# Kernel tuning notes

Measured on AMD Instinct MI355X. Metric: run time of the kernel, lower is better.

## Reference

```python
import jax, jax.numpy as jnp
import numpy as np

N = 12        # ALL_QUBITS
COM_Q = 9     # COM_QUBITS
IMG_Q = 11    # IMG_QUBITS
LAYERS = 2
SQRT2 = float(np.sqrt(2.0))
H_GATE = jnp.asarray([[1.0, 1.0], [1.0, -1.0]], dtype=jnp.complex64) / SQRT2


def _bitrev_perm(q):
    # column j of the wires-1..q subspace corresponds to param index bitrev(j)
    idx = np.arange(2 ** q)
    rev = np.zeros_like(idx)
    for bpos in range(q):
        rev |= ((idx >> bpos) & 1) << (q - 1 - bpos)
    return rev


def _apply_1q(state, U, w):
    # state: (B, 2^N) complex; apply 2x2 gate U on wire w (wire 0 = MSB)
    B = state.shape[0]
    s = state.reshape(B, 2 ** w, 2, -1)
    return jnp.einsum('ij,bpjq->bpiq', U, s).reshape(B, -1)


def _apply_cnot(state, c, t):
    B = state.shape[0]
    s = state.reshape((B,) + (2,) * N)
    s0 = jax.lax.slice_in_dim(s, 0, 1, axis=c + 1)
    s1 = jnp.flip(jax.lax.slice_in_dim(s, 1, 2, axis=c + 1), axis=t + 1)
    return jnp.concatenate([s0, s1], axis=c + 1).reshape(B, -1)


def _frqi(state, angles, q):
    # Hadamards on wires 1..q, then uniformly-controlled RY(angles) on wire 0
    for w in range(1, q + 1):
        state = _apply_1q(state, H_GATE, w)
    rev = _bitrev_perm(q)
    half = 0.5 * angles[:, rev]            # (B, 2^q), angle per control column
    c = jnp.cos(half)[:, :, None]
    s = jnp.sin(half)[:, :, None]
    B = state.shape[0]
    st = state.reshape(B, 2, 2 ** q, -1)   # (B, wire0, wires1..q, rest)
    new0 = c * st[:, 0] - s * st[:, 1]
    new1 = s * st[:, 0] + c * st[:, 1]
    return jnp.stack([new0, new1], axis=1).reshape(B, -1)


def _rot(phi, theta, omega):
    # PennyLane Rot = RZ(omega) RY(theta) RZ(phi)
    c = jnp.cos(theta / 2)
    s = jnp.sin(theta / 2)
    m00 = jnp.exp(-0.5j * (phi + omega)) * c
    m01 = -jnp.exp(0.5j * (phi - omega)) * s
    m10 = jnp.exp(-0.5j * (phi - omega)) * s
    m11 = jnp.exp(0.5j * (phi + omega)) * c
    return jnp.stack([jnp.stack([m00, m01]), jnp.stack([m10, m11])])


def _circuit(com_params, img_params, qp):
    B = com_params.shape[0]
    state = jnp.zeros((B, 2 ** N), jnp.complex64).at[:, 0].set(1.0)
    state = _frqi(state, com_params, COM_Q)
    for l in range(LAYERS):  # StronglyEntanglingLayers
        for w in range(N):
            state = _apply_1q(state, _rot(qp[l, w, 0], qp[l, w, 1], qp[l, w, 2]), w)
        r = l % (N - 1) + 1  # default ranges
        for w in range(N):
            state = _apply_cnot(state, w, (w + r) % N)
    state = _frqi(state, img_params, IMG_Q)
    p = (jnp.abs(state.reshape(B, 2, -1)) ** 2).sum(axis=2)  # (B, 2) wire-0 probs
    return p[:, 1] - p[:, 0]  # expval of Hamiltonian = -1 * Z(0)


def setup_inputs() -> dict:
    key = jax.random.key(0)
    k1, k2, k3 = jax.random.split(key, 3)
    B = 1024
    x = jax.random.uniform(k1, (B, 2, 32, 32), dtype=jnp.float32)
    W = jax.random.normal(k2, (512, 2048), dtype=jnp.float32) * 0.02
    b = jnp.zeros((512,), dtype=jnp.float32)
    quantum_params = jax.random.uniform(k3, (LAYERS, N, 3), dtype=jnp.float32) * float(np.pi)
    return {"x": x, "W": W, "b": b, "quantum_params": quantum_params}


def reference(x, W, b, quantum_params):
    B = x.shape[0]
    xf = x.reshape(B, -1)                 # (B, 2048) img_params
    com = xf @ W.T + b                    # (B, 512) classical_nn output
    return _circuit(com, xf, quantum_params)
```

## Files before the change

### kernel.cpp

```cpp
#include <hip/hip_runtime.h>
#include <math.h>

#define RS2f 0.70710678118654752f
#define XSTR 4160

typedef __attribute__((ext_vector_type(8))) short bf16x8;
typedef __attribute__((ext_vector_type(4))) float f32x4;

__device__ __forceinline__ unsigned short f2bf(float f) {
    unsigned u = __float_as_uint(f);
    unsigned r = (u + 0x7fffu + ((u >> 16) & 1u)) >> 16;
    return (unsigned short)r;
}
__device__ __forceinline__ float bf2f(unsigned short h) {
    return __uint_as_float(((unsigned)h) << 16);
}

__global__ __launch_bounds__(256) void split_all(const float* __restrict__ x,
                                                 const float* __restrict__ W,
                                                 unsigned short* __restrict__ xc,
                                                 unsigned short* __restrict__ wc) {
    int idx = blockIdx.x * 256 + threadIdx.x;
    const float* src; unsigned short* dst;
    if (idx < 524288) { src = x; dst = xc; }
    else              { idx -= 524288; src = W; dst = wc; }
    int m = idx >> 9;
    int c4 = (idx & 511) << 2;
    const float4 v = *(const float4*)&src[m * 2048 + c4];
    ushort4 hi, lo;
    hi.x = f2bf(v.x); lo.x = f2bf(v.x - bf2f(hi.x));
    hi.y = f2bf(v.y); lo.y = f2bf(v.y - bf2f(hi.y));
    hi.z = f2bf(v.z); lo.z = f2bf(v.z - bf2f(hi.z));
    hi.w = f2bf(v.w); lo.w = f2bf(v.w - bf2f(hi.w));
    *(ushort4*)&dst[(size_t)m * XSTR + c4] = hi;
    *(ushort4*)&dst[(size_t)m * XSTR + 2048 + c4] = lo;
}

__global__ __launch_bounds__(256) void gemm64(const unsigned short* __restrict__ A,
                                              const unsigned short* __restrict__ B,
                                              float* __restrict__ P, int nch) {
    __shared__ short As[64 * 64];
    __shared__ short Bs[64 * 64];
    const int tid = threadIdx.x, lane = tid & 63, wv = tid >> 6;
    const int quad = lane >> 4, mrow = lane & 15;
    const int m0 = blockIdx.x * 64, n0 = blockIdx.y * 64;
    const int kb = blockIdx.z * nch * 64;
    const int lrow = lane >> 3;
    const int gseg = (lane & 7) ^ lrow;

    f32x4 acc[4];
    #pragma unroll
    for (int j = 0; j < 4; ++j) acc[j] = (f32x4){0.f, 0.f, 0.f, 0.f};

    for (int ch = 0; ch < nch; ++ch) {
        const int ko = kb + ch * 64;
        #pragma unroll
        for (int t = 0; t < 2; ++t) {
            const int ra = (wv * 2 + t) * 8;
            const unsigned short* ga = A + (size_t)(m0 + ra + lrow) * XSTR + ko + gseg * 8;
            const unsigned short* gb = B + (size_t)(n0 + ra + lrow) * XSTR + ko + gseg * 8;
            __builtin_amdgcn_global_load_lds(
                (const __attribute__((address_space(1))) void*)ga,
                (__attribute__((address_space(3))) void*)(As + ra * 64), 16, 0, 0);
            __builtin_amdgcn_global_load_lds(
                (const __attribute__((address_space(1))) void*)gb,
                (__attribute__((address_space(3))) void*)(Bs + ra * 64), 16, 0, 0);
        }
        __syncthreads();
        #pragma unroll
        for (int ks = 0; ks < 2; ++ks) {
            const int q = ks * 4 + quad;
            const int am = wv * 16 + mrow;
            bf16x8 af = *(const bf16x8*)&As[am * 64 + ((q ^ (am & 7)) << 3)];
            #pragma unroll
            for (int j = 0; j < 4; ++j) {
                const int bn = j * 16 + mrow;
                bf16x8 bf = *(const bf16x8*)&Bs[bn * 64 + ((q ^ (bn & 7)) << 3)];
                acc[j] = __builtin_amdgcn_mfma_f32_16x16x32_bf16(af, bf, acc[j], 0, 0, 0);
            }
        }
        __syncthreads();
    }
    float* Pz = P + (size_t)blockIdx.z * 524288;
    #pragma unroll
    for (int j = 0; j < 4; ++j)
        #pragma unroll
        for (int r = 0; r < 4; ++r)
            Pz[(m0 + wv * 16 + quad * 4 + r) * 512 + n0 + j * 16 + mrow] = acc[j][r];
}

__global__ __launch_bounds__(256) void reduce_kernel(float* __restrict__ P,
                                                     const float* __restrict__ bias,
                                                     int SK) {
    int i = blockIdx.x * 256 + threadIdx.x;
    float s = bias[i & 511];
    for (int z = 0; z < SK; ++z) s += P[(size_t)z * 524288 + i];
    P[i] = s;
}

__global__ __launch_bounds__(256) void gemm_f32(const float* __restrict__ A,
                                                const float* __restrict__ W,
                                                float* __restrict__ C) {
    __shared__ float Asf[64][33];
    __shared__ float Bsf[32][33];
    const int tid = threadIdx.x;
    const int m0 = blockIdx.x * 64;
    const int n0 = blockIdx.y * 32;
    const int tm = tid >> 4, tn = tid & 15;
    float acc[4][2] = {};
    for (int k0 = 0; k0 < 2048; k0 += 32) {
        #pragma unroll
        for (int i = 0; i < 8; ++i) {
            int idx = tid + i * 256;
            Asf[idx >> 5][idx & 31] = A[(m0 + (idx >> 5)) * 2048 + k0 + (idx & 31)];
        }
        #pragma unroll
        for (int i = 0; i < 4; ++i) {
            int idx = tid + i * 256;
            Bsf[idx >> 5][idx & 31] = W[(n0 + (idx >> 5)) * 2048 + k0 + (idx & 31)];
        }
        __syncthreads();
        #pragma unroll
        for (int kk = 0; kk < 32; ++kk) {
            float a0 = Asf[tm*4+0][kk], a1 = Asf[tm*4+1][kk];
            float a2 = Asf[tm*4+2][kk], a3 = Asf[tm*4+3][kk];
            float b0 = Bsf[tn*2+0][kk], b1 = Bsf[tn*2+1][kk];
            acc[0][0] += a0*b0; acc[0][1] += a0*b1;
            acc[1][0] += a1*b0; acc[1][1] += a1*b1;
            acc[2][0] += a2*b0; acc[2][1] += a2*b1;
            acc[3][0] += a3*b0; acc[3][1] += a3*b1;
        }
        __syncthreads();
    }
    #pragma unroll
    for (int r = 0; r < 4; ++r)
        #pragma unroll
        for (int c = 0; c < 2; ++c)
            C[(m0 + tm*4 + r) * 512 + n0 + tn*2 + c] = acc[r][c];
}

struct CMat { float m00r,m00i,m01r,m01i,m10r,m10i,m11r,m11i; };

__device__ __forceinline__ CMat mk_rot(const float* __restrict__ qp, int l, int w) {
    const float* g = qp + (l * 12 + w) * 3;
    float phi = g[0], th = g[1], om = g[2];
    float st, ct, sa, ca, sb, cb;
    sincosf(0.5f * th, &st, &ct);
    sincosf(0.5f * (phi + om), &sa, &ca);
    sincosf(0.5f * (phi - om), &sb, &cb);
    CMat M;
    M.m00r =  ct * ca; M.m00i = -ct * sa;
    M.m01r = -st * cb; M.m01i = -st * sb;
    M.m10r =  st * cb; M.m10i = -st * sb;
    M.m11r =  ct * ca; M.m11i =  ct * sa;
    return M;
}

template<int W> struct WI {
    static constexpr int kind = (W == 0 || W == 7) ? 2 : ((W >= 1 && W <= 6) ? 1 : 0);
    static constexpr int eb   = (W >= 8) ? (11 - W) : 0;
    static constexpr int lm   = (W >= 1 && W <= 6) ? (1 << (6 - W)) : 0;
    static constexpr int vm   = (W == 0) ? 2 : ((W == 7) ? 1 : 0);
};

__device__ __forceinline__ void exch_put(float* xbuf, int slot,
                                         const float vr[16], const float vi[16]) {
    __syncthreads();
    float4* p = (float4*)xbuf;
    #pragma unroll
    for (int j = 0; j < 8; ++j)
        p[(j << 8) + slot] = make_float4(vr[2*j], vi[2*j], vr[2*j+1], vi[2*j+1]);
    __syncthreads();
}

__device__ __forceinline__ void shfl_perm(float vr[16], float vi[16], int src) {
    #pragma unroll
    for (int e = 0; e < 16; ++e) {
        vr[e] = __shfl(vr[e], src, 64);
        vi[e] = __shfl(vi[e], src, 64);
    }
}

template<int EB>
__device__ __forceinline__ void rot_local(float vr[16], float vi[16], const CMat& M) {
    #pragma unroll
    for (int e = 0; e < 16; ++e) if (!(e & (1 << EB))) {
        const int e1 = e | (1 << EB);
        float x0r = vr[e],  x0i = vi[e];
        float x1r = vr[e1], x1i = vi[e1];
        vr[e]  = M.m00r*x0r - M.m00i*x0i + M.m01r*x1r - M.m01i*x1i;
        vi[e]  = M.m00r*x0i + M.m00i*x0r + M.m01r*x1i + M.m01i*x1r;
        vr[e1] = M.m10r*x0r - M.m10i*x0i + M.m11r*x1r - M.m11i*x1i;
        vi[e1] = M.m10r*x0i + M.m10i*x0r + M.m11r*x1i + M.m11i*x1r;
    }
}

template<int LM>
__device__ __forceinline__ void rot_lane(float vr[16], float vi[16], int lane, const CMat& M) {
    const bool hi = lane & LM;
    const float Ar = hi ? M.m11r : M.m00r, Ai = hi ? M.m11i : M.m00i;
    const float Br = hi ? M.m10r : M.m01r, Bi = hi ? M.m10i : M.m01i;
    #pragma unroll
    for (int e = 0; e < 16; ++e) {
        float pr = __shfl_xor(vr[e], LM, 64);
        float pi = __shfl_xor(vi[e], LM, 64);
        float orr = vr[e], oi = vi[e];
        vr[e] = Ar*orr - Ai*oi + Br*pr - Bi*pi;
        vi[e] = Ar*oi + Ai*orr + Br*pi + Bi*pr;
    }
}

template<int VM>
__device__ __forceinline__ void rot_wave(float vr[16], float vi[16], float* xbuf,
                                         int waveId, int lane, const CMat& M) {
    exch_put(xbuf, (waveId << 6) + lane, vr, vi);
    const float4* p = (const float4*)xbuf;
    const int ps = ((waveId ^ VM) << 6) + lane;
    const bool hi = waveId & VM;
    const float Ar = hi ? M.m11r : M.m00r, Ai = hi ? M.m11i : M.m00i;
    const float Br = hi ? M.m10r : M.m01r, Bi = hi ? M.m10i : M.m01i;
    #pragma unroll
    for (int j = 0; j < 8; ++j) {
        float4 q = p[(j << 8) + ps];
        const int e0 = 2*j, e1 = 2*j + 1;
        float r0 = vr[e0], i0 = vi[e0], r1 = vr[e1], i1 = vi[e1];
        vr[e0] = Ar*r0 - Ai*i0 + Br*q.x - Bi*q.y;
        vi[e0] = Ar*i0 + Ai*r0 + Br*q.y + Bi*q.x;
        vr[e1] = Ar*r1 - Ai*i1 + Br*q.z - Bi*q.w;
        vi[e1] = Ar*i1 + Ai*r1 + Br*q.w + Bi*q.z;
    }
}

template<int W>
__device__ __forceinline__ void rot_wire(float vr[16], float vi[16], float* xbuf,
                                         int waveId, int lane, const CMat& M) {
    if constexpr (WI<W>::kind == 0)      rot_local<WI<W>::eb>(vr, vi, M);
    else if constexpr (WI<W>::kind == 1) rot_lane<WI<W>::lm>(vr, vi, lane, M);
    else                                 rot_wave<WI<W>::vm>(vr, vi, xbuf, waveId, lane, M);
}

template<int C, int T>
__device__ __forceinline__ void cnot(float vr[16], float vi[16], float* xbuf,
                                     int waveId, int lane) {
    constexpr int ck = WI<C>::kind, tk = WI<T>::kind;
    if constexpr (ck == 0 && tk == 0) {
        constexpr int cb = 1 << WI<C>::eb, tb = 1 << WI<T>::eb;
        #pragma unroll
        for (int e = 0; e < 16; ++e) if ((e & cb) && !(e & tb)) {
            const int e1 = e | tb;
            float t = vr[e]; vr[e] = vr[e1]; vr[e1] = t;
            t = vi[e]; vi[e] = vi[e1]; vi[e1] = t;
        }
    } else if constexpr (ck == 0 && tk == 1) {
        constexpr int cb = 1 << WI<C>::eb, tm = WI<T>::lm;
        #pragma unroll
        for (int e = 0; e < 16; ++e) if (e & cb) {
            vr[e] = __shfl_xor(vr[e], tm, 64);
            vi[e] = __shfl_xor(vi[e], tm, 64);
        }
    } else if constexpr (ck == 0 && tk == 2) {
        constexpr int cb = 1 << WI<C>::eb, vm = WI<T>::vm;
        exch_put(xbuf, (waveId << 6) + lane, vr, vi);
        const float4* p = (const float4*)xbuf;
        const int ps = ((waveId ^ vm) << 6) + lane;
        #pragma unroll
        for (int j = 0; j < 8; ++j) {
            if ((((2*j) & cb) != 0) || (((2*j+1) & cb) != 0)) {
                float4 q = p[(j << 8) + ps];
                if (((2*j) & cb) != 0)   { vr[2*j]   = q.x; vi[2*j]   = q.y; }
                if (((2*j+1) & cb) != 0) { vr[2*j+1] = q.z; vi[2*j+1] = q.w; }
            }
        }
    } else if constexpr (ck == 1 && tk == 0) {
        constexpr int cm = WI<C>::lm, tb = 1 << WI<T>::eb;
        const bool cc = lane & cm;
        #pragma unroll
        for (int e = 0; e < 16; ++e) if (!(e & tb)) {
            const int e1 = e | tb;
            float a = vr[e], bb = vr[e1];
            vr[e] = cc ? bb : a; vr[e1] = cc ? a : bb;
            a = vi[e]; bb = vi[e1];
            vi[e] = cc ? bb : a; vi[e1] = cc ? a : bb;
        }
    } else if constexpr (ck == 1 && tk == 1) {
        constexpr int cm = WI<C>::lm, tm = WI<T>::lm;
        const int src = (lane & cm) ? (lane ^ tm) : lane;
        shfl_perm(vr, vi, src);
    } else if constexpr (ck == 1 && tk == 2) {
        constexpr int cm = WI<C>::lm, vm = WI<T>::vm;
        exch_put(xbuf, (waveId << 6) + lane, vr, vi);
        const float4* p = (const float4*)xbuf;
        const int ps = ((waveId ^ vm) << 6) + lane;
        const bool take = lane & cm;
        #pragma unroll
        for (int j = 0; j < 8; ++j) {
            float4 q = p[(j << 8) + ps];
            vr[2*j]   = take ? q.x : vr[2*j];   vi[2*j]   = take ? q.y : vi[2*j];
            vr[2*j+1] = take ? q.z : vr[2*j+1]; vi[2*j+1] = take ? q.w : vi[2*j+1];
        }
    } else if constexpr (ck == 2 && tk == 0) {
        constexpr int vm = WI<C>::vm, tb = 1 << WI<T>::eb;
        if (waveId & vm) {
            #pragma unroll
            for (int e = 0; e < 16; ++e) if (!(e & tb)) {
                const int e1 = e | tb;
                float t = vr[e]; vr[e] = vr[e1]; vr[e1] = t;
                t = vi[e]; vi[e] = vi[e1]; vi[e1] = t;
            }
        }
    } else {
        constexpr int vm = WI<C>::vm, tm = WI<T>::lm;
        if (waveId & vm) {
            #pragma unroll
            for (int e = 0; e < 16; ++e) {
                vr[e] = __shfl_xor(vr[e], tm, 64);
                vi[e] = __shfl_xor(vi[e], tm, 64);
            }
        }
    }
}

template<int W>
__device__ __forceinline__ void h_wire(float vr[16], float vi[16], float* xbuf,
                                       int waveId, int lane) {
    if constexpr (WI<W>::kind == 0) {
        constexpr int tb = 1 << WI<W>::eb;
        #pragma unroll
        for (int e = 0; e < 16; ++e) if (!(e & tb)) {
            const int e1 = e | tb;
            float x0 = vr[e], x1 = vr[e1];
            vr[e] = (x0 + x1) * RS2f; vr[e1] = (x0 - x1) * RS2f;
            x0 = vi[e]; x1 = vi[e1];
            vi[e] = (x0 + x1) * RS2f; vi[e1] = (x0 - x1) * RS2f;
        }
    } else if constexpr (WI<W>::kind == 1) {
        constexpr int m = WI<W>::lm;
        const float sgn = (lane & m) ? -RS2f : RS2f;
        #pragma unroll
        for (int e = 0; e < 16; ++e) {
            float pr = __shfl_xor(vr[e], m, 64);
            float pi = __shfl_xor(vi[e], m, 64);
            vr[e] = pr * RS2f + vr[e] * sgn;
            vi[e] = pi * RS2f + vi[e] * sgn;
        }
    } else {
        constexpr int vm = WI<W>::vm;
        exch_put(xbuf, (waveId << 6) + lane, vr, vi);
        const float4* p = (const float4*)xbuf;
        const int ps = ((waveId ^ vm) << 6) + lane;
        const float sgn = (waveId & vm) ? -RS2f : RS2f;
        #pragma unroll
        for (int j = 0; j < 8; ++j) {
            float4 q = p[(j << 8) + ps];
            vr[2*j]   = q.x * RS2f + vr[2*j]   * sgn;
            vi[2*j]   = q.y * RS2f + vi[2*j]   * sgn;
            vr[2*j+1] = q.z * RS2f + vr[2*j+1] * sgn;
            vi[2*j+1] = q.w * RS2f + vi[2*j+1] * sgn;
        }
    }
}

__global__ __launch_bounds__(256) void circuit_sa(const float* __restrict__ com,
                                                  const float* __restrict__ xf,
                                                  const float* __restrict__ qp,
                                                  float* __restrict__ out) {
    __shared__ float xbuf[8192];
    __shared__ float ang[2048];
    const int tid = threadIdx.x, lane = tid & 63, waveId = tid >> 6;
    const int b = blockIdx.x;
    if (tid < 128) ((float4*)ang)[tid] = ((const float4*)(com + b * 512))[tid];
    __syncthreads();
    float vr[16], vi[16];
    #pragma unroll
    for (int e = 0; e < 16; ++e) { vr[e] = 0.0f; vi[e] = 0.0f; }
    const float K9 = 0.044194173824159216f;
    #pragma unroll
    for (int m = 0; m < 4; ++m) {
        int j = (lane << 3) | ((waveId & 1) << 2) | m;
        int rj = (int)(__brev((unsigned)j) >> 23);
        float s, c;
        sincosf(0.5f * ang[rj], &s, &c);
        vr[m << 2] = K9 * ((waveId & 2) ? s : c);
    }
    #pragma unroll 1
    for (int l = 0; l < 2; ++l) {
        { CMat M = mk_rot(qp, l, 0);  rot_wire<0 >(vr, vi, xbuf, waveId, lane, M); }
        { CMat M = mk_rot(qp, l, 1);  rot_wire<1 >(vr, vi, xbuf, waveId, lane, M); }
        { CMat M = mk_rot(qp, l, 2);  rot_wire<2 >(vr, vi, xbuf, waveId, lane, M); }
        { CMat M = mk_rot(qp, l, 3);  rot_wire<3 >(vr, vi, xbuf, waveId, lane, M); }
        { CMat M = mk_rot(qp, l, 4);  rot_wire<4 >(vr, vi, xbuf, waveId, lane, M); }
        { CMat M = mk_rot(qp, l, 5);  rot_wire<5 >(vr, vi, xbuf, waveId, lane, M); }
        { CMat M = mk_rot(qp, l, 6);  rot_wire<6 >(vr, vi, xbuf, waveId, lane, M); }
        { CMat M = mk_rot(qp, l, 7);  rot_wire<7 >(vr, vi, xbuf, waveId, lane, M); }
        { CMat M = mk_rot(qp, l, 8);  rot_wire<8 >(vr, vi, xbuf, waveId, lane, M); }
        { CMat M = mk_rot(qp, l, 9);  rot_wire<9 >(vr, vi, xbuf, waveId, lane, M); }
        { CMat M = mk_rot(qp, l, 10); rot_wire<10>(vr, vi, xbuf, waveId, lane, M); }
        { CMat M = mk_rot(qp, l, 11); rot_wire<11>(vr, vi, xbuf, waveId, lane, M); }
        if (l == 0) {
            int j = lane;
            j ^= (j & 2)  ? 1  : 0;
            j ^= (j & 4)  ? 2  : 0;
            j ^= (j & 8)  ? 4  : 0;
            j ^= (j & 16) ? 8  : 0;
            j ^= (j & 32) ? 16 : 0;
            j ^= (waveId & 2) ? 32 : 0;
            shfl_perm(vr, vi, j);
            cnot<6,7>(vr,vi,xbuf,waveId,lane);   cnot<7,8>(vr,vi,xbuf,waveId,lane);
            cnot<8,9>(vr,vi,xbuf,waveId,lane);   cnot<9,10>(vr,vi,xbuf,waveId,lane);
            cnot<10,11>(vr,vi,xbuf,waveId,lane); cnot<11,0>(vr,vi,xbuf,waveId,lane);
        } else {
            int j = lane;
            j ^= (j & 4)  ? 1  : 0;
            j ^= (j & 8)  ? 2  : 0;
            j ^= (j & 16) ? 4  : 0;
            j ^= (j & 32) ? 8  : 0;
            j ^= (waveId & 2) ? 16 : 0;
            shfl_perm(vr, vi, j);
            cnot<5,7>(vr,vi,xbuf,waveId,lane);   cnot<6,8>(vr,vi,xbuf,waveId,lane);
            cnot<7,9>(vr,vi,xbuf,waveId,lane);   cnot<8,10>(vr,vi,xbuf,waveId,lane);
            cnot<9,11>(vr,vi,xbuf,waveId,lane);  cnot<10,0>(vr,vi,xbuf,waveId,lane);
            cnot<11,1>(vr,vi,xbuf,waveId,lane);
        }
    }
    h_wire<1>(vr,vi,xbuf,waveId,lane);  h_wire<2>(vr,vi,xbuf,waveId,lane);
    h_wire<3>(vr,vi,xbuf,waveId,lane);  h_wire<4>(vr,vi,xbuf,waveId,lane);
    h_wire<5>(vr,vi,xbuf,waveId,lane);  h_wire<6>(vr,vi,xbuf,waveId,lane);
    h_wire<7>(vr,vi,xbuf,waveId,lane);  h_wire<8>(vr,vi,xbuf,waveId,lane);
    h_wire<9>(vr,vi,xbuf,waveId,lane);  h_wire<10>(vr,vi,xbuf,waveId,lane);
    h_wire<11>(vr,vi,xbuf,waveId,lane);
    {
        const float4* x4 = (const float4*)(xf + b * 2048);
        ((float4*)ang)[tid]       = x4[tid];
        ((float4*)ang)[tid + 256] = x4[tid + 256];
    }
    __syncthreads();
    exch_put(xbuf, (waveId << 6) + lane, vr, vi);
    {
        const float4* p = (const float4*)xbuf;
        const int ps = ((waveId ^ 2) << 6) + lane;
        const bool hi = waveId & 2;
        float acc = 0.0f;
        #pragma unroll
        for (int j = 0; j < 8; ++j) {
            float4 q = p[(j << 8) + ps];
            #pragma unroll
            for (int h = 0; h < 2; ++h) {
                const int e = 2*j + h;
                const float prr = h ? q.z : q.x;
                const float pii = h ? q.w : q.y;
                int v = (lane << 5) | ((waveId & 1) << 4) | e;
                int rv = (int)(__brev((unsigned)v) >> 21);
                float s, c;
                sincosf(0.5f * ang[rv], &s, &c);
                float nr = hi ? (s*prr + c*vr[e]) : (c*vr[e] - s*prr);
                float ni = hi ? (s*pii + c*vi[e]) : (c*vi[e] - s*pii);
                acc += nr*nr + ni*ni;
            }
        }
        if (!hi) acc = -acc;
        #pragma unroll
        for (int off = 32; off > 0; off >>= 1) acc += __shfl_down(acc, off, 64);
        __syncthreads();
        if (lane == 0) xbuf[waveId] = acc;
        __syncthreads();
        if (tid == 0) out[b] = xbuf[0] + xbuf[1] + xbuf[2] + xbuf[3];
    }
}

extern "C" void kernel_launch(void* const* d_in, const int* in_sizes, int n_in,
                              void* d_out, int out_size, void* d_ws, size_t ws_size,
                              hipStream_t stream) {
    const float* x    = (const float*)d_in[0];
    const float* W    = (const float*)d_in[1];
    const float* bias = (const float*)d_in[2];
    const float* qp   = (const float*)d_in[3];
    float* out = (float*)d_out;

    const size_t XC = (size_t)1024 * XSTR * 2;
    const size_t WC = (size_t)512 * XSTR * 2;
    const size_t SLAB = 2097152;
    const size_t BASE = XC + WC;
    if (ws_size >= BASE + SLAB) {
        unsigned short* xc = (unsigned short*)d_ws;
        unsigned short* wc = (unsigned short*)((char*)d_ws + XC);
        float* P = (float*)((char*)d_ws + BASE);
        int SK = 1;
        if      (ws_size >= BASE + 8 * SLAB) SK = 8;
        else if (ws_size >= BASE + 4 * SLAB) SK = 4;
        else if (ws_size >= BASE + 2 * SLAB) SK = 2;
        split_all<<<3072, 256, 0, stream>>>(x, W, xc, wc);
        dim3 g(16, 8, SK);
        gemm64<<<g, 256, 0, stream>>>(xc, wc, P, 64 / SK);
        reduce_kernel<<<2048, 256, 0, stream>>>(P, bias, SK);
        circuit_sa<<<1024, 256, 0, stream>>>(P, x, qp, out);
    } else {
        float* P = (float*)d_ws;
        dim3 g(16, 16);
        gemm_f32<<<g, 256, 0, stream>>>(x, W, P);
        reduce_kernel<<<2048, 256, 0, stream>>>(P, bias, 1);
        circuit_sa<<<1024, 256, 0, stream>>>(P, x, qp, out);
    }
}
```

Before: 151.7 us.

## Fuse bf16 hi/lo split into GEMM with register prefetch of next K chunk

Drops the separate split_all kernel and its workspace round trip: the GEMM now loads fp32 x and W directly, converts them to bf16 hi/lo pairs in registers and writes both halves into padded shared-memory tiles. The next K chunk is prefetched into registers while MFMAs run on the current tile. Split-K drops from up to 8 to at most 4, which means fewer blocks and more conversion work inside each block. The padded LDS layout replaces the XOR swizzle.

```diff
diff --git a/kernel.cpp b/kernel.cpp
--- a/kernel.cpp
+++ b/kernel.cpp
@@ -2,7 +2,6 @@
 #include <math.h>
 
 #define RS2f 0.70710678118654752f
-#define XSTR 4160
 
 typedef __attribute__((ext_vector_type(8))) short bf16x8;
 typedef __attribute__((ext_vector_type(4))) float f32x4;
@@ -16,70 +15,65 @@
     return __uint_as_float(((unsigned)h) << 16);
 }
 
-__global__ __launch_bounds__(256) void split_all(const float* __restrict__ x,
-                                                 const float* __restrict__ W,
-                                                 unsigned short* __restrict__ xc,
-                                                 unsigned short* __restrict__ wc) {
-    int idx = blockIdx.x * 256 + threadIdx.x;
-    const float* src; unsigned short* dst;
-    if (idx < 524288) { src = x; dst = xc; }
-    else              { idx -= 524288; src = W; dst = wc; }
-    int m = idx >> 9;
-    int c4 = (idx & 511) << 2;
-    const float4 v = *(const float4*)&src[m * 2048 + c4];
-    ushort4 hi, lo;
-    hi.x = f2bf(v.x); lo.x = f2bf(v.x - bf2f(hi.x));
-    hi.y = f2bf(v.y); lo.y = f2bf(v.y - bf2f(hi.y));
-    hi.z = f2bf(v.z); lo.z = f2bf(v.z - bf2f(hi.z));
-    hi.w = f2bf(v.w); lo.w = f2bf(v.w - bf2f(hi.w));
-    *(ushort4*)&dst[(size_t)m * XSTR + c4] = hi;
-    *(ushort4*)&dst[(size_t)m * XSTR + 2048 + c4] = lo;
-}
-
-__global__ __launch_bounds__(256) void gemm64(const unsigned short* __restrict__ A,
-                                              const unsigned short* __restrict__ B,
-                                              float* __restrict__ P, int nch) {
-    __shared__ short As[64 * 64];
-    __shared__ short Bs[64 * 64];
+__global__ __launch_bounds__(256) void gemm_fused(const float* __restrict__ A,
+                                                  const float* __restrict__ B,
+                                                  float* __restrict__ P, int nch) {
+    __shared__ short As[64 * 136];
+    __shared__ short Bs[64 * 136];
     const int tid = threadIdx.x, lane = tid & 63, wv = tid >> 6;
     const int quad = lane >> 4, mrow = lane & 15;
     const int m0 = blockIdx.x * 64, n0 = blockIdx.y * 64;
     const int kb = blockIdx.z * nch * 64;
-    const int lrow = lane >> 3;
-    const int gseg = (lane & 7) ^ lrow;
+    const int srow = tid >> 2;
+    const int sc = (tid & 3) * 16;
 
     f32x4 acc[4];
     #pragma unroll
     for (int j = 0; j < 4; ++j) acc[j] = (f32x4){0.f, 0.f, 0.f, 0.f};
 
+    const float* Arow = A + (size_t)(m0 + srow) * 2048 + kb + sc;
+    const float* Brow = B + (size_t)(n0 + srow) * 2048 + kb + sc;
+
+    float4 av[4], bv[4];
+    #pragma unroll
+    for (int i = 0; i < 4; ++i) { av[i] = *(const float4*)(Arow + 4*i);
+                                  bv[i] = *(const float4*)(Brow + 4*i); }
+
     for (int ch = 0; ch < nch; ++ch) {
-        const int ko = kb + ch * 64;
-        #pragma unroll
-        for (int t = 0; t < 2; ++t) {
-            const int ra = (wv * 2 + t) * 8;
-            const unsigned short* ga = A + (size_t)(m0 + ra + lrow) * XSTR + ko + gseg * 8;
-            const unsigned short* gb = B + (size_t)(n0 + ra + lrow) * XSTR + ko + gseg * 8;
-            __builtin_amdgcn_global_load_lds(
-                (const __attribute__((address_space(1))) void*)ga,
-                (__attribute__((address_space(3))) void*)(As + ra * 64), 16, 0, 0);
-            __builtin_amdgcn_global_load_lds(
-                (const __attribute__((address_space(1))) void*)gb,
-                (__attribute__((address_space(3))) void*)(Bs + ra * 64), 16, 0, 0);
-        }
-        __syncthreads();
-        #pragma unroll
-        for (int ks = 0; ks < 2; ++ks) {
-            const int q = ks * 4 + quad;
-            const int am = wv * 16 + mrow;
-            bf16x8 af = *(const bf16x8*)&As[am * 64 + ((q ^ (am & 7)) << 3)];
+        __syncthreads();
+        #pragma unroll
+        for (int i = 0; i < 4; ++i) {
+            ushort4 hi, lo;
+            hi.x = f2bf(av[i].x); lo.x = f2bf(av[i].x - bf2f(hi.x));
+            hi.y = f2bf(av[i].y); lo.y = f2bf(av[i].y - bf2f(hi.y));
+            hi.z = f2bf(av[i].z); lo.z = f2bf(av[i].z - bf2f(hi.z));
+            hi.w = f2bf(av[i].w); lo.w = f2bf(av[i].w - bf2f(hi.w));
+            *(ushort4*)&As[srow * 136 + sc + 4*i]      = hi;
+            *(ushort4*)&As[srow * 136 + 64 + sc + 4*i] = lo;
+            hi.x = f2bf(bv[i].x); lo.x = f2bf(bv[i].x - bf2f(hi.x));
+            hi.y = f2bf(bv[i].y); lo.y = f2bf(bv[i].y - bf2f(hi.y));
+            hi.z = f2bf(bv[i].z); lo.z = f2bf(bv[i].z - bf2f(hi.z));
+            hi.w = f2bf(bv[i].w); lo.w = f2bf(bv[i].w - bf2f(hi.w));
+            *(ushort4*)&Bs[srow * 136 + sc + 4*i]      = hi;
+            *(ushort4*)&Bs[srow * 136 + 64 + sc + 4*i] = lo;
+        }
+        __syncthreads();
+        if (ch + 1 < nch) {
+            const int o = (ch + 1) * 64;
+            #pragma unroll
+            for (int i = 0; i < 4; ++i) { av[i] = *(const float4*)(Arow + o + 4*i);
+                                          bv[i] = *(const float4*)(Brow + o + 4*i); }
+        }
+        #pragma unroll
+        for (int s = 0; s < 4; ++s) {
+            const int off = s * 32 + quad * 8;
+            bf16x8 af = *(const bf16x8*)&As[(wv * 16 + mrow) * 136 + off];
             #pragma unroll
             for (int j = 0; j < 4; ++j) {
-                const int bn = j * 16 + mrow;
-                bf16x8 bf = *(const bf16x8*)&Bs[bn * 64 + ((q ^ (bn & 7)) << 3)];
+                bf16x8 bf = *(const bf16x8*)&Bs[(j * 16 + mrow) * 136 + off];
                 acc[j] = __builtin_amdgcn_mfma_f32_16x16x32_bf16(af, bf, acc[j], 0, 0, 0);
             }
         }
-        __syncthreads();
     }
     float* Pz = P + (size_t)blockIdx.z * 524288;
     #pragma unroll
@@ -476,25 +470,15 @@
     const float* qp   = (const float*)d_in[3];
     float* out = (float*)d_out;
 
-    const size_t XC = (size_t)1024 * XSTR * 2;
-    const size_t WC = (size_t)512 * XSTR * 2;
     const size_t SLAB = 2097152;
-    const size_t BASE = XC + WC;
-    if (ws_size >= BASE + SLAB) {
-        unsigned short* xc = (unsigned short*)d_ws;
-        unsigned short* wc = (unsigned short*)((char*)d_ws + XC);
-        float* P = (float*)((char*)d_ws + BASE);
-        int SK = 1;
-        if      (ws_size >= BASE + 8 * SLAB) SK = 8;
-        else if (ws_size >= BASE + 4 * SLAB) SK = 4;
-        else if (ws_size >= BASE + 2 * SLAB) SK = 2;
-        split_all<<<3072, 256, 0, stream>>>(x, W, xc, wc);
+    float* P = (float*)d_ws;
+    if (ws_size >= 2 * SLAB) {
+        int SK = (ws_size >= 4 * SLAB) ? 4 : 2;
         dim3 g(16, 8, SK);
-        gemm64<<<g, 256, 0, stream>>>(xc, wc, P, 64 / SK);
+        gemm_fused<<<g, 256, 0, stream>>>(x, W, P, 32 / SK);
         reduce_kernel<<<2048, 256, 0, stream>>>(P, bias, SK);
         circuit_sa<<<1024, 256, 0, stream>>>(P, x, qp, out);
     } else {
-        float* P = (float*)d_ws;
         dim3 g(16, 16);
         gemm_f32<<<g, 256, 0, stream>>>(x, W, P);
         reduce_kernel<<<2048, 256, 0, stream>>>(P, bias, 1);
```

New measurement: 149.1 us. Within noise of the previous version (-1.7%).
